# Kernel optimization log

Measured on AMD Instinct MI355X. Metric: run time of the kernel, lower is better.

The kernel has to match this reference:

```python
import jax, jax.numpy as jnp
import numpy as np

N = 50000
E = 800000
IN_DIM, HID, OUT, DW = 128, 96, 40, 64
N_LBL = 10


def _deg_inv_sqrt(dst, n):
    # PyG gcn_norm: degree over target nodes of (A + I)
    deg = jax.ops.segment_sum(jnp.ones((dst.shape[0],), jnp.float32), dst, num_segments=n) + 1.0
    return jnp.where(deg > 0, 1.0 / jnp.sqrt(deg), 0.0)


def gcn_conv(h_in, W, b, src, dst, dinv):
    # GCNConv: out = D^-1/2 (A + I) D^-1/2 (X W) + b
    h = h_in @ W                                  # [N, F]
    norm = (dinv[src] * dinv[dst])[:, None]       # [E, 1]
    agg = jax.ops.segment_sum(h[src] * norm, dst, num_segments=h.shape[0])
    agg = agg + h * (dinv * dinv)[:, None]        # self-loop term
    return agg + b


def setup_inputs() -> dict:
    key = jax.random.key(0)
    ks = jax.random.split(key, 12)
    inp = {
        "x": jax.random.normal(ks[0], (N, IN_DIM), jnp.float32),
        "y": jax.random.uniform(ks[1], (N, OUT), jnp.float32),
        "edge_index": jax.random.randint(ks[2], (2, E), 0, N, jnp.int64 if jax.config.read("jax_enable_x64") else jnp.int32),
        "deep_walk_emb": jax.random.normal(ks[3], (N, DW), jnp.float32),
        # learned params
        "W_gcn1": jax.random.normal(ks[4], (IN_DIM, HID), jnp.float32) * (1.0 / np.sqrt(IN_DIM)),
        "b_gcn1": jnp.zeros((HID,), jnp.float32),
        "W_gcn2": jax.random.normal(ks[5], (HID, HID), jnp.float32) * (1.0 / np.sqrt(HID)),
        "b_gcn2": jnp.zeros((HID,), jnp.float32),
        "W_lbl": jax.random.normal(ks[6], (N_LBL, OUT, OUT), jnp.float32) * (1.0 / np.sqrt(OUT)),
        "b_lbl": jnp.zeros((N_LBL, OUT), jnp.float32),
        "W_fuse": jax.random.normal(ks[7], (HID + OUT + DW, OUT), jnp.float32) * (1.0 / np.sqrt(HID + OUT + DW)),
        "b_fuse": jnp.zeros((OUT,), jnp.float32),
    }
    return inp


def reference(x, y, edge_index, deep_walk_emb,
              W_gcn1, b_gcn1, W_gcn2, b_gcn2,
              W_lbl, b_lbl, W_fuse, b_fuse):
    src, dst = edge_index[0], edge_index[1]
    dinv = _deg_inv_sqrt(dst, x.shape[0])

    # feature propagation: 2 stacked GCNConv layers
    h = gcn_conv(x, W_gcn1, b_gcn1, src, dst, dinv)
    h = gcn_conv(h, W_gcn2, b_gcn2, src, dst, dinv)

    # label propagation: 10 stacked GCNConv layers via scan over stacked weights
    def step(carry, wb):
        W, b = wb
        return gcn_conv(carry, W, b, src, dst, dinv), None

    x_label, _ = jax.lax.scan(step, y, (W_lbl, b_lbl))

    fused = jnp.concatenate([h, x_label, deep_walk_emb], axis=1)  # [N, HID+OUT+DW]
    out = fused @ W_fuse + b_fuse
    return jax.nn.sigmoid(out)
```

## Files before the change

### kernel.cpp

```cpp
#include <hip/hip_runtime.h>
#include <hip/hip_bf16.h>
#include <math.h>

#define THREADS 256
typedef _Float16 h16;

__device__ __forceinline__ void ld8h(const h16* p, float* f) {
    union { uint4 u; h16 h[8]; } c;
    c.u = *(const uint4*)p;
#pragma unroll
    for (int j = 0; j < 8; ++j) f[j] = (float)c.h[j];
}

__global__ __launch_bounds__(256) void count_part_kernel(
    const int* __restrict__ dst, int* __restrict__ cnt, int E, int n)
{
    const int cls = blockIdx.x & 7;
    const int nb  = gridDim.x >> 3;
    const int sub = blockIdx.x >> 3;
    const int lo = (int)((long long)n * cls / 8);
    const int hi = (int)((long long)n * (cls + 1) / 8);
    const int stride = nb * 256;
    for (int e = sub * 256 + threadIdx.x; e < E; e += stride) {
        int d = dst[e];
        if (d >= lo && d < hi) atomicAdd(&cnt[d], 1);
    }
}

__global__ __launch_bounds__(256) void scatter_part_kernel(
    const int* __restrict__ src, const int* __restrict__ dst,
    int* __restrict__ cursor, int* __restrict__ col, int E, int n)
{
    const int cls = blockIdx.x & 7;
    const int nb  = gridDim.x >> 3;
    const int sub = blockIdx.x >> 3;
    const int lo = (int)((long long)n * cls / 8);
    const int hi = (int)((long long)n * (cls + 1) / 8);
    const int stride = nb * 256;
    for (int e = sub * 256 + threadIdx.x; e < E; e += stride) {
        int d = dst[e];
        if (d >= lo && d < hi) {
            int p = atomicAdd(&cursor[d], 1);
            col[p] = src[e];
        }
    }
}

__global__ __launch_bounds__(256) void scanp1_pre_kernel(
    const int* __restrict__ cnt, int* __restrict__ partial, int n, int NB,
    const float* __restrict__ Wl, const float* __restrict__ bl,
    const float* __restrict__ W1, const float* __restrict__ W2,
    const float* __restrict__ b1,
    float* __restrict__ C0, float* __restrict__ betas,
    float* __restrict__ W12, float* __restrict__ betaf1)
{
    __shared__ __align__(16) float smem[9216];
    const int tid = threadIdx.x;
    const int bid = blockIdx.x;

    if (bid < NB) {
        int* red = (int*)smem;
        int base = bid * 1024 + tid * 4;
        int s = 0;
        if (base + 3 < n) {
            int4 v = *(const int4*)(cnt + base);
            s = v.x + v.y + v.z + v.w;
        } else {
            for (int k = 0; k < 4; k++) { int i = base + k; if (i < n) s += cnt[i]; }
        }
        red[tid] = s;
        __syncthreads();
        for (int off = 128; off > 0; off >>= 1) {
            if (tid < off) red[tid] += red[tid + off];
            __syncthreads();
        }
        if (tid == 0) partial[bid] = red[0];
        return;
    }

    if (bid == NB) {
        float* Ca  = smem;
        float* Cb  = smem + 1600;
        float* sWm = smem + 3200;
        float* bls = smem + 4800;
        for (int idx = tid; idx < 100; idx += 256)
            ((float4*)bls)[idx] = ((const float4*)bl)[idx];
        for (int idx = tid; idx < 1600; idx += 256)
            Ca[idx] = ((idx / 40) == (idx % 40)) ? 1.f : 0.f;
        if (tid < 40) betas[9 * 40 + tid] = bl[9 * 40 + tid];
        __syncthreads();
        float* cur = Ca;
        float* nxt = Cb;
        for (int m = 9; m >= 0; --m) {
            for (int idx = tid; idx < 400; idx += 256)
                ((float4*)sWm)[idx] = ((const float4*)(Wl + (size_t)m * 1600))[idx];
            __syncthreads();
            for (int sid = tid; sid < 400; sid += 256) {
                int i = sid / 10, jq = sid - (sid / 10) * 10;
                const float* wr = &sWm[i * 40];
                const float4* c4 = (const float4*)cur;
                float4 a = make_float4(0.f, 0.f, 0.f, 0.f);
#pragma unroll
                for (int k = 0; k < 40; ++k) {
                    float w = wr[k];
                    float4 c = c4[k * 10 + jq];
                    a.x = fmaf(w, c.x, a.x); a.y = fmaf(w, c.y, a.y);
                    a.z = fmaf(w, c.z, a.z); a.w = fmaf(w, c.w, a.w);
                }
                ((float4*)nxt)[sid] = a;
            }
            __syncthreads();
            if (m >= 1 && tid < 40) {
                float s = 0.f;
                const float* br = &bls[(m - 1) * 40];
#pragma unroll
                for (int k = 0; k < 40; ++k) s = fmaf(br[k], nxt[k * 40 + tid], s);
                betas[(size_t)(m - 1) * 40 + tid] = s;
            }
            float* t = cur; cur = nxt; nxt = t;
            __syncthreads();
        }
        for (int idx = tid; idx < 1600; idx += 256) C0[idx] = cur[idx];
        return;
    }

    float* sW2 = smem;
    for (int idx = tid; idx < 2304; idx += 256)
        ((float4*)sW2)[idx] = ((const float4*)W2)[idx];
    __syncthreads();
    int idx = (bid - NB - 1) * 256 + tid;
    {
        int i = idx / 96, j = idx - (idx / 96) * 96;
        float s = 0.f;
        const float* wr = W1 + (size_t)i * 96;
#pragma unroll 8
        for (int k = 0; k < 96; ++k) s = fmaf(wr[k], sW2[k * 96 + j], s);
        W12[idx] = s;
    }
    if (bid == NB + 1 && tid < 96) {
        float s = 0.f;
        for (int k = 0; k < 96; ++k) s = fmaf(b1[k], sW2[k * 96 + tid], s);
        betaf1[tid] = s;
    }
}

__global__ __launch_bounds__(256) void scan_p2(int* __restrict__ partial, int* __restrict__ rowptr, int nb, int n) {
    __shared__ int sm[256];
    int tid = threadIdx.x;
    int v = (tid < nb) ? partial[tid] : 0;
    sm[tid] = v;
    __syncthreads();
    int acc = v;
    for (int off = 1; off < 256; off <<= 1) {
        int t = (tid >= off) ? sm[tid - off] : 0;
        __syncthreads();
        acc += t;
        sm[tid] = acc;
        __syncthreads();
    }
    if (tid < nb) partial[tid] = acc - v;
    if (tid == 255) rowptr[n] = sm[255];
}

__global__ __launch_bounds__(256) void scan_p3(const int* __restrict__ cnt, const int* __restrict__ partial,
                                               int* __restrict__ rowptr, int* __restrict__ cursor,
                                               float* __restrict__ dinv, int n) {
    __shared__ int tsum[256];
    int tid = threadIdx.x;
    int base = blockIdx.x * 1024 + tid * 4;
    int v0 = 0, v1 = 0, v2 = 0, v3 = 0;
    if (base + 3 < n) {
        int4 t = *(const int4*)(cnt + base);
        v0 = t.x; v1 = t.y; v2 = t.z; v3 = t.w;
    } else {
        if (base + 0 < n) v0 = cnt[base + 0];
        if (base + 1 < n) v1 = cnt[base + 1];
        if (base + 2 < n) v2 = cnt[base + 2];
        if (base + 3 < n) v3 = cnt[base + 3];
    }
    int s = v0 + v1 + v2 + v3;
    tsum[tid] = s;
    __syncthreads();
    int acc = s;
    for (int off = 1; off < 256; off <<= 1) {
        int t = (tid >= off) ? tsum[tid - off] : 0;
        __syncthreads();
        acc += t;
        tsum[tid] = acc;
        __syncthreads();
    }
    int run = partial[blockIdx.x] + acc - s;
    int vv[4] = {v0, v1, v2, v3};
    for (int k = 0; k < 4; k++) {
        int i = base + k;
        if (i < n) {
            rowptr[i] = run; cursor[i] = run; run += vv[k];
            dinv[i] = rsqrtf((float)vv[k] + 1.0f);
        }
    }
}

template<int FIN, int FOUT, typename TX>
__device__ __forceinline__ void gemm_body(
    const TX* __restrict__ X, const float* __restrict__ W,
    const float* __restrict__ dinv, h16* __restrict__ Y, int n,
    float* sX, float* sW, int bid, int tid)
{
    constexpr int KC = (FIN % 32 == 0) ? 32 : FIN;
    constexpr int NCHUNK = FIN / KC;
    constexpr int TN = (FOUT + 15) / 16;
    constexpr int BM = 64;
    constexpr int KP = KC + 4;

    const int tj = tid & 15;
    const int ti = tid >> 4;
    const int i0 = bid * BM;

    float acc[4][TN] = {};

    for (int c = 0; c < NCHUNK; ++c) {
        const int k0 = c * KC;
        __syncthreads();
        if constexpr (sizeof(TX) == 2) {
            constexpr int K8 = KC / 8;
            for (int v = tid; v < BM * K8; v += 256) {
                int r = v / K8, q = v - r * K8;
                int gi = i0 + r;
                float f[8] = {0.f, 0.f, 0.f, 0.f, 0.f, 0.f, 0.f, 0.f};
                if (gi < n) ld8h((const h16*)X + (size_t)gi * FIN + k0 + q * 8, f);
                float* p = &sX[r * KP + q * 8];
#pragma unroll
                for (int j = 0; j < 8; ++j) p[j] = f[j];
            }
        } else {
            constexpr int K4 = KC / 4;
            for (int v = tid; v < BM * K4; v += 256) {
                int r = v / K4, q = v - r * K4;
                int gi = i0 + r;
                float4 val = (gi < n) ? *(const float4*)((const float*)X + (size_t)gi * FIN + k0 + q * 4)
                                      : make_float4(0.f, 0.f, 0.f, 0.f);
                float* p = &sX[r * KP + q * 4];
                p[0] = val.x; p[1] = val.y; p[2] = val.z; p[3] = val.w;
            }
        }
        for (int v = tid; v < KC * FOUT; v += 256) {
            int kk = v / FOUT;
            int j = v - kk * FOUT;
            sW[j * KP + kk] = W[(size_t)(k0 + kk) * FOUT + j];
        }
        __syncthreads();
#pragma unroll
        for (int kk = 0; kk < KC; kk += 4) {
            float4 xv[4];
#pragma unroll
            for (int m = 0; m < 4; ++m)
                xv[m] = *(const float4*)&sX[(ti + 16 * m) * KP + kk];
#pragma unroll
            for (int u = 0; u < TN; ++u) {
                float4 wv = *(const float4*)&sW[(tj + 16 * u) * KP + kk];
#pragma unroll
                for (int m = 0; m < 4; ++m) {
                    acc[m][u] = fmaf(xv[m].x, wv.x, acc[m][u]);
                    acc[m][u] = fmaf(xv[m].y, wv.y, acc[m][u]);
                    acc[m][u] = fmaf(xv[m].z, wv.z, acc[m][u]);
                    acc[m][u] = fmaf(xv[m].w, wv.w, acc[m][u]);
                }
            }
        }
    }

#pragma unroll
    for (int m = 0; m < 4; ++m) {
        int gi = i0 + ti + 16 * m;
        if (gi >= n) continue;
        float dv = dinv[gi];
#pragma unroll
        for (int u = 0; u < TN; ++u) {
            int j = tj + 16 * u;
            if (j < FOUT) Y[(size_t)gi * FOUT + j] = (h16)(acc[m][u] * dv);
        }
    }
}

template<int FIN, int FOUT, typename TX>
__global__ __launch_bounds__(256) void gemm_kernel(
    const TX* __restrict__ X, const float* __restrict__ W,
    const float* __restrict__ dinv, h16* __restrict__ Y, int n)
{
    constexpr int KC = (FIN % 32 == 0) ? 32 : FIN;
    constexpr int KP = KC + 4;
    constexpr int TN = (FOUT + 15) / 16;
    __shared__ __align__(16) float smem[64 * KP + TN * 16 * KP];
    gemm_body<FIN, FOUT, TX>(X, W, dinv, Y, n, smem, smem + 64 * KP, blockIdx.x, threadIdx.x);
}

template<int F, int PRE>
__device__ __forceinline__ void agg_body(
    const h16* __restrict__ hs, const int* __restrict__ rowptr,
    const int* __restrict__ col, const float* __restrict__ dinv,
    const float* __restrict__ bias, h16* __restrict__ out, int n,
    int bid, int tid)
{
    constexpr int F8 = F / 8;
    int gt = bid * 256 + tid;
    if (gt >= n * F8) return;
    int i = gt / F8;
    int f = gt - i * F8;
    int s = rowptr[i], e = rowptr[i + 1];
    const h16* base = hs + (size_t)f * 8;
    float acc[8];
    ld8h(hs + (size_t)i * F + f * 8, acc);
    int k = s;
    for (; k + 8 <= e; k += 8) {
        int c[8];
        union { uint4 u; h16 h[8]; } a[8];
#pragma unroll
        for (int q = 0; q < 8; ++q) c[q] = col[k + q];
#pragma unroll
        for (int q = 0; q < 8; ++q) a[q].u = *(const uint4*)(base + (size_t)c[q] * F);
#pragma unroll
        for (int j = 0; j < 8; ++j) {
            float t0 = ((float)a[0].h[j] + (float)a[1].h[j]) + ((float)a[2].h[j] + (float)a[3].h[j]);
            float t1 = ((float)a[4].h[j] + (float)a[5].h[j]) + ((float)a[6].h[j] + (float)a[7].h[j]);
            acc[j] += t0 + t1;
        }
    }
    for (; k + 4 <= e; k += 4) {
        int c0 = col[k], c1 = col[k + 1], c2 = col[k + 2], c3 = col[k + 3];
        union { uint4 u; h16 h[8]; } a0, a1, a2, a3;
        a0.u = *(const uint4*)(base + (size_t)c0 * F);
        a1.u = *(const uint4*)(base + (size_t)c1 * F);
        a2.u = *(const uint4*)(base + (size_t)c2 * F);
        a3.u = *(const uint4*)(base + (size_t)c3 * F);
#pragma unroll
        for (int j = 0; j < 8; ++j)
            acc[j] += ((float)a0.h[j] + (float)a1.h[j]) + ((float)a2.h[j] + (float)a3.h[j]);
    }
    for (; k < e; k++) {
        float v[8];
        ld8h(base + (size_t)col[k] * F, v);
#pragma unroll
        for (int j = 0; j < 8; ++j) acc[j] += v[j];
    }
    float dv = dinv[i];
    float sc = PRE ? dv : 1.f;
    union { uint4 u; h16 h[8]; } o;
#pragma unroll
    for (int j = 0; j < 8; ++j) o.h[j] = (h16)((acc[j] * dv + bias[f * 8 + j]) * sc);
    *(uint4*)(out + (size_t)i * F + f * 8) = o.u;
}

template<int F, int PRE>
__global__ __launch_bounds__(256) void agg_h(
    const h16* __restrict__ hs, const int* __restrict__ rowptr,
    const int* __restrict__ col, const float* __restrict__ dinv,
    const float* __restrict__ bias, h16* __restrict__ out, int n) {
    agg_body<F, PRE>(hs, rowptr, col, dinv, bias, out, n, blockIdx.x, threadIdx.x);
}

template<int PRE2>
__global__ __launch_bounds__(256) void agg_dual_kernel(
    const h16* __restrict__ hsA, const float* __restrict__ biasA, h16* __restrict__ outA,
    const h16* __restrict__ hsB, const float* __restrict__ biasB, h16* __restrict__ outB,
    const int* __restrict__ rowptr, const int* __restrict__ col,
    const float* __restrict__ dinv, int n, int nblkA)
{
    if (blockIdx.x < nblkA)
        agg_body<40, 1>(hsA, rowptr, col, dinv, biasA, outA, n, blockIdx.x, threadIdx.x);
    else
        agg_body<96, PRE2>(hsB, rowptr, col, dinv, biasB, outB, n, blockIdx.x - nblkA, threadIdx.x);
}

template<int KC, typename T>
__device__ __forceinline__ void fuse_chunk(
    const T* __restrict__ src, int FIN, int k0, int wrow0,
    const float* __restrict__ Wf, float* sX, float* sW,
    float acc[4][3], int i0, int n, int tid)
{
    constexpr int KP = 44;
    __syncthreads();
    if constexpr (sizeof(T) == 2) {
        constexpr int K8 = KC / 8;
        for (int v = tid; v < 64 * K8; v += 256) {
            int r = v / K8, q = v - r * K8;
            int gi = i0 + r;
            float f[8] = {0.f, 0.f, 0.f, 0.f, 0.f, 0.f, 0.f, 0.f};
            if (gi < n) ld8h((const h16*)src + (size_t)gi * FIN + k0 + q * 8, f);
            float* p = &sX[r * KP + q * 8];
#pragma unroll
            for (int j = 0; j < 8; ++j) p[j] = f[j];
        }
    } else {
        constexpr int K4 = KC / 4;
        for (int v = tid; v < 64 * K4; v += 256) {
            int r = v / K4, q = v - r * K4;
            int gi = i0 + r;
            float4 val = (gi < n) ? *(const float4*)((const float*)src + (size_t)gi * FIN + k0 + q * 4)
                                  : make_float4(0.f, 0.f, 0.f, 0.f);
            float* p = &sX[r * KP + q * 4];
            p[0] = val.x; p[1] = val.y; p[2] = val.z; p[3] = val.w;
        }
    }
    for (int v = tid; v < KC * 40; v += 256) {
        int kk = v / 40, j = v - kk * 40;
        sW[j * KP + kk] = Wf[(size_t)(wrow0 + kk) * 40 + j];
    }
    __syncthreads();
    int tj = tid & 15, ti = tid >> 4;
#pragma unroll
    for (int kk = 0; kk < KC; kk += 4) {
        float4 xv[4];
#pragma unroll
        for (int m = 0; m < 4; ++m)
            xv[m] = *(const float4*)&sX[(ti + 16 * m) * KP + kk];
#pragma unroll
        for (int u = 0; u < 3; ++u) {
            float4 wv = *(const float4*)&sW[(tj + 16 * u) * KP + kk];
#pragma unroll
            for (int m = 0; m < 4; ++m) {
                acc[m][u] = fmaf(xv[m].x, wv.x, acc[m][u]);
                acc[m][u] = fmaf(xv[m].y, wv.y, acc[m][u]);
                acc[m][u] = fmaf(xv[m].z, wv.z, acc[m][u]);
                acc[m][u] = fmaf(xv[m].w, wv.w, acc[m][u]);
            }
        }
    }
}

__global__ __launch_bounds__(256) void fuse_gemm_kernel(
    const h16* __restrict__ h2, const h16* __restrict__ xl,
    const float* __restrict__ dw, const float* __restrict__ Wf,
    const float* __restrict__ bf, float* __restrict__ out, int n)
{
    __shared__ __align__(16) float sX[64 * 44];
    __shared__ __align__(16) float sW[48 * 44];
    float acc[4][3] = {};
    const int tid = threadIdx.x;
    const int i0 = blockIdx.x * 64;
    fuse_chunk<32>(h2, 96, 0,  0,   Wf, sX, sW, acc, i0, n, tid);
    fuse_chunk<32>(h2, 96, 32, 32,  Wf, sX, sW, acc, i0, n, tid);
    fuse_chunk<32>(h2, 96, 64, 64,  Wf, sX, sW, acc, i0, n, tid);
    fuse_chunk<40>(xl, 40, 0,  96,  Wf, sX, sW, acc, i0, n, tid);
    fuse_chunk<32>(dw, 64, 0,  136, Wf, sX, sW, acc, i0, n, tid);
    fuse_chunk<32>(dw, 64, 32, 168, Wf, sX, sW, acc, i0, n, tid);
    const int tj = tid & 15, ti = tid >> 4;
#pragma unroll
    for (int m = 0; m < 4; ++m) {
        int gi = i0 + ti + 16 * m;
        if (gi >= n) continue;
#pragma unroll
        for (int u = 0; u < 3; ++u) {
            int j = tj + 16 * u;
            if (j < 40) {
                float t = acc[m][u] + bf[j];
                out[(size_t)gi * 40 + j] = 1.f / (1.f + expf(-t));
            }
        }
    }
}

extern "C" void kernel_launch(void* const* d_in, const int* in_sizes, int n_in,
                              void* d_out, int out_size, void* d_ws, size_t ws_size,
                              hipStream_t stream) {
    const float* x   = (const float*)d_in[0];
    const float* y   = (const float*)d_in[1];
    const int*   ei  = (const int*)d_in[2];
    const float* dwe = (const float*)d_in[3];
    const float* W1  = (const float*)d_in[4];
    const float* b1  = (const float*)d_in[5];
    const float* W2  = (const float*)d_in[6];
    const float* b2  = (const float*)d_in[7];
    const float* Wl  = (const float*)d_in[8];
    const float* bl  = (const float*)d_in[9];
    const float* Wf  = (const float*)d_in[10];
    const float* bf  = (const float*)d_in[11];
    float* out = (float*)d_out;

    const int n = in_sizes[0] / 128;
    const int E = in_sizes[2] / 2;
    const int* srcp = ei;
    const int* dstp = ei + E;

    char* ws = (char*)d_ws;
    size_t off = 0;
    auto alloc = [&](size_t bytes) -> void* {
        void* p = ws + off;
        off += bytes;
        off = (off + 255) & ~(size_t)255;
        return p;
    };

    int*   cnt     = (int*)alloc((size_t)n * 4);
    float* dinv    = (float*)alloc((size_t)n * 4);
    int*   rowptr  = (int*)alloc((size_t)(n + 1) * 4);
    int*   cursor  = (int*)alloc((size_t)n * 4);
    int*   partial = (int*)alloc(256 * 4);
    int*   col     = (int*)alloc((size_t)E * 4);
    h16*   A96     = (h16*)alloc((size_t)n * 96 * 2);
    h16*   B96     = (h16*)alloc((size_t)n * 96 * 2);
    h16*   Z0      = (h16*)alloc((size_t)n * 40 * 2);
    h16*   LA      = (h16*)alloc((size_t)n * 40 * 2);
    h16*   LB      = (h16*)alloc((size_t)n * 40 * 2);
    float* C0      = (float*)alloc(1600 * 4);
    float* betas   = (float*)alloc(10 * 40 * 4);
    float* W12     = (float*)alloc(128 * 96 * 4);
    float* betaf1  = (float*)alloc(96 * 4);
    (void)ws_size;

    const int NB      = (n + 1023) / 1024;
    const int gb_gm   = (n + 63) / 64;
    const int gb_a96  = (n * 12 + THREADS - 1) / THREADS;
    const int gb_a40  = (n * 5 + THREADS - 1) / THREADS;
    const int PART_BLOCKS = 2048;

    hipMemsetAsync(cnt, 0, (size_t)n * 4, stream);
    count_part_kernel<<<PART_BLOCKS, THREADS, 0, stream>>>(dstp, cnt, E, n);
    scanp1_pre_kernel<<<NB + 49, THREADS, 0, stream>>>(
        cnt, partial, n, NB, Wl, bl, W1, W2, b1, C0, betas, W12, betaf1);
    scan_p2<<<1, THREADS, 0, stream>>>(partial, rowptr, NB, n);
    scan_p3<<<NB, THREADS, 0, stream>>>(cnt, partial, rowptr, cursor, dinv, n);
    scatter_part_kernel<<<PART_BLOCKS, THREADS, 0, stream>>>(srcp, dstp, cursor, col, E, n);

    gemm_kernel<40, 40, float><<<gb_gm, THREADS, 0, stream>>>(y, C0, dinv, Z0, n);
    gemm_kernel<128, 96, float><<<gb_gm, THREADS, 0, stream>>>(x, W12, dinv, A96, n);

    agg_dual_kernel<1><<<gb_a40 + gb_a96, THREADS, 0, stream>>>(
        Z0, betas + 0, LA, A96, betaf1, B96, rowptr, col, dinv, n, gb_a40);
    agg_dual_kernel<0><<<gb_a40 + gb_a96, THREADS, 0, stream>>>(
        LA, betas + 40, LB, B96, b2, A96, rowptr, col, dinv, n, gb_a40);

    const h16* cur = LB;
    const h16* xl = LB;
    for (int m = 3; m <= 10; m++) {
        h16* nxt = (m & 1) ? LA : LB;
        if (m < 10)
            agg_h<40, 1><<<gb_a40, THREADS, 0, stream>>>(cur, rowptr, col, dinv, betas + (size_t)(m - 1) * 40, nxt, n);
        else
            agg_h<40, 0><<<gb_a40, THREADS, 0, stream>>>(cur, rowptr, col, dinv, betas + (size_t)(m - 1) * 40, nxt, n);
        cur = nxt;
        xl = nxt;
    }

    fuse_gemm_kernel<<<gb_gm, THREADS, 0, stream>>>(A96, xl, dwe, Wf, bf, out, n);
}
```

Measured before the change: 386.5 us.

## Merge aggregation layers into one cooperative persistent kernel with grid syncs

Replaces ten separate aggregation kernel launches (two dual-feature and eight label-propagation launches) with a single cooperative kernel. It uses a persistent grid sized from occupancy and separates layers with grid.sync(). The aim is to cut per-launch overhead and the gaps between dependent layers. The cost is grid-wide barrier latency, possibly lower occupancy, and a grid-stride loop over work blocks.

```diff
diff --git a/kernel.cpp b/kernel.cpp
--- a/kernel.cpp
+++ b/kernel.cpp
@@ -1,6 +1,9 @@
 #include <hip/hip_runtime.h>
 #include <hip/hip_bf16.h>
+#include <hip/hip_cooperative_groups.h>
 #include <math.h>
+
+namespace cg = cooperative_groups;
 
 #define THREADS 256
 typedef _Float16 h16;
@@ -350,25 +353,41 @@
     *(uint4*)(out + (size_t)i * F + f * 8) = o.u;
 }
 
-template<int F, int PRE>
-__global__ __launch_bounds__(256) void agg_h(
-    const h16* __restrict__ hs, const int* __restrict__ rowptr,
-    const int* __restrict__ col, const float* __restrict__ dinv,
-    const float* __restrict__ bias, h16* __restrict__ out, int n) {
-    agg_body<F, PRE>(hs, rowptr, col, dinv, bias, out, n, blockIdx.x, threadIdx.x);
-}
-
-template<int PRE2>
-__global__ __launch_bounds__(256) void agg_dual_kernel(
-    const h16* __restrict__ hsA, const float* __restrict__ biasA, h16* __restrict__ outA,
-    const h16* __restrict__ hsB, const float* __restrict__ biasB, h16* __restrict__ outB,
+__global__ __launch_bounds__(256) void agg_coop_kernel(
+    const h16* __restrict__ Z0, h16* __restrict__ LA, h16* __restrict__ LB,
+    h16* __restrict__ A96, h16* __restrict__ B96,
+    const float* __restrict__ betas, const float* __restrict__ betaf1,
+    const float* __restrict__ b2,
     const int* __restrict__ rowptr, const int* __restrict__ col,
-    const float* __restrict__ dinv, int n, int nblkA)
-{
-    if (blockIdx.x < nblkA)
-        agg_body<40, 1>(hsA, rowptr, col, dinv, biasA, outA, n, blockIdx.x, threadIdx.x);
-    else
-        agg_body<96, PRE2>(hsB, rowptr, col, dinv, biasB, outB, n, blockIdx.x - nblkA, threadIdx.x);
+    const float* __restrict__ dinv, int n, int nblkL, int nblkF)
+{
+    cg::grid_group grid = cg::this_grid();
+    const int G = gridDim.x;
+    const int tid = threadIdx.x;
+
+    for (int w = blockIdx.x; w < nblkL + nblkF; w += G) {
+        if (w < nblkL) agg_body<40, 1>(Z0, rowptr, col, dinv, betas, LA, n, w, tid);
+        else           agg_body<96, 1>(A96, rowptr, col, dinv, betaf1, B96, n, w - nblkL, tid);
+    }
+    grid.sync();
+    for (int w = blockIdx.x; w < nblkL + nblkF; w += G) {
+        if (w < nblkL) agg_body<40, 1>(LA, rowptr, col, dinv, betas + 40, LB, n, w, tid);
+        else           agg_body<96, 0>(B96, rowptr, col, dinv, b2, A96, n, w - nblkL, tid);
+    }
+    const h16* cur = LB;
+    for (int m = 3; m <= 10; ++m) {
+        grid.sync();
+        h16* nxt = (m & 1) ? LA : LB;
+        const float* beta = betas + (size_t)(m - 1) * 40;
+        if (m < 10) {
+            for (int w = blockIdx.x; w < nblkL; w += G)
+                agg_body<40, 1>(cur, rowptr, col, dinv, beta, nxt, n, w, tid);
+        } else {
+            for (int w = blockIdx.x; w < nblkL; w += G)
+                agg_body<40, 0>(cur, rowptr, col, dinv, beta, nxt, n, w, tid);
+        }
+        cur = nxt;
+    }
 }
 
 template<int KC, typename T>
@@ -524,22 +543,30 @@
     gemm_kernel<40, 40, float><<<gb_gm, THREADS, 0, stream>>>(y, C0, dinv, Z0, n);
     gemm_kernel<128, 96, float><<<gb_gm, THREADS, 0, stream>>>(x, W12, dinv, A96, n);
 
-    agg_dual_kernel<1><<<gb_a40 + gb_a96, THREADS, 0, stream>>>(
-        Z0, betas + 0, LA, A96, betaf1, B96, rowptr, col, dinv, n, gb_a40);
-    agg_dual_kernel<0><<<gb_a40 + gb_a96, THREADS, 0, stream>>>(
-        LA, betas + 40, LB, B96, b2, A96, rowptr, col, dinv, n, gb_a40);
-
-    const h16* cur = LB;
-    const h16* xl = LB;
-    for (int m = 3; m <= 10; m++) {
-        h16* nxt = (m & 1) ? LA : LB;
-        if (m < 10)
-            agg_h<40, 1><<<gb_a40, THREADS, 0, stream>>>(cur, rowptr, col, dinv, betas + (size_t)(m - 1) * 40, nxt, n);
-        else
-            agg_h<40, 0><<<gb_a40, THREADS, 0, stream>>>(cur, rowptr, col, dinv, betas + (size_t)(m - 1) * 40, nxt, n);
-        cur = nxt;
-        xl = nxt;
-    }
-
-    fuse_gemm_kernel<<<gb_gm, THREADS, 0, stream>>>(A96, xl, dwe, Wf, bf, out, n);
-}
+    {
+        int perCU = 0;
+        hipError_t oe = hipOccupancyMaxActiveBlocksPerMultiprocessor(
+            &perCU, (const void*)agg_coop_kernel, THREADS, 0);
+        if (oe != hipSuccess || perCU <= 0) perCU = 4;
+        int grid = perCU * 256;
+        int maxwork = gb_a40 + gb_a96;
+        if (grid > maxwork) grid = maxwork;
+
+        const h16* z0c = Z0;
+        h16 *laP = LA, *lbP = LB, *a96P = A96, *b96P = B96;
+        const float *betasP = betas, *betaf1P = betaf1, *b2P = b2;
+        const int *rowptrP = rowptr, *colP = col;
+        const float* dinvP = dinv;
+        int nv = n, nblkL = gb_a40, nblkF = gb_a96;
+        void* cargs[] = {
+            (void*)&z0c, (void*)&laP, (void*)&lbP, (void*)&a96P, (void*)&b96P,
+            (void*)&betasP, (void*)&betaf1P, (void*)&b2P,
+            (void*)&rowptrP, (void*)&colP, (void*)&dinvP,
+            (void*)&nv, (void*)&nblkL, (void*)&nblkF
+        };
+        hipLaunchCooperativeKernel((const void*)agg_coop_kernel,
+                                   dim3(grid), dim3(THREADS), cargs, 0, stream);
+    }
+
+    fuse_gemm_kernel<<<gb_gm, THREADS, 0, stream>>>(A96, LB, dwe, Wf, bf, out, n);
+}
```

Result: slower. 982.4 us (+154.2%).

## Fold fusion weights into GCN chains so all propagation runs at width 40

Applied to the files above, without the earlier changes.

Pushes the final fusion matrix Wf back through both linear chains. The feature path is precomputed as W1·W2·Wf1, and the label chain product is folded into Wf's label block, so both GCN branches aggregate 40-wide half-precision features instead of 96-wide. The deepwalk projection is done by a separate small GEMM and added during the second hop, and the final fusion GEMM is replaced by a sigmoid epilogue in the last aggregation. This cuts gather bandwidth and removes the fuse kernel, at the cost of a longer serial weight-precompute block and changed rounding order.

```diff
diff --git a/kernel.cpp b/kernel.cpp
--- a/kernel.cpp
+++ b/kernel.cpp
@@ -49,12 +49,12 @@
 __global__ __launch_bounds__(256) void scanp1_pre_kernel(
     const int* __restrict__ cnt, int* __restrict__ partial, int n, int NB,
     const float* __restrict__ Wl, const float* __restrict__ bl,
-    const float* __restrict__ W1, const float* __restrict__ W2,
-    const float* __restrict__ b1,
-    float* __restrict__ C0, float* __restrict__ betas,
-    float* __restrict__ W12, float* __restrict__ betaf1)
-{
-    __shared__ __align__(16) float smem[9216];
+    const float* __restrict__ W2, const float* __restrict__ b1,
+    const float* __restrict__ b2, const float* __restrict__ Wf,
+    float* __restrict__ CM, float* __restrict__ betas,
+    float* __restrict__ T, float* __restrict__ betaf1p, float* __restrict__ b2p)
+{
+    __shared__ __align__(16) float smem[13200];
     const int tid = threadIdx.x;
     const int bid = blockIdx.x;
 
@@ -78,88 +78,121 @@
         return;
     }
 
-    if (bid == NB) {
-        float* Ca  = smem;
-        float* Cb  = smem + 1600;
-        float* sWm = smem + 3200;
-        float* bls = smem + 4800;
-        for (int idx = tid; idx < 100; idx += 256)
-            ((float4*)bls)[idx] = ((const float4*)bl)[idx];
-        for (int idx = tid; idx < 1600; idx += 256)
-            Ca[idx] = ((idx / 40) == (idx % 40)) ? 1.f : 0.f;
-        if (tid < 40) betas[9 * 40 + tid] = bl[9 * 40 + tid];
-        __syncthreads();
-        float* cur = Ca;
-        float* nxt = Cb;
-        for (int m = 9; m >= 0; --m) {
-            for (int idx = tid; idx < 400; idx += 256)
-                ((float4*)sWm)[idx] = ((const float4*)(Wl + (size_t)m * 1600))[idx];
-            __syncthreads();
-            for (int sid = tid; sid < 400; sid += 256) {
-                int i = sid / 10, jq = sid - (sid / 10) * 10;
-                const float* wr = &sWm[i * 40];
-                const float4* c4 = (const float4*)cur;
-                float4 a = make_float4(0.f, 0.f, 0.f, 0.f);
-#pragma unroll
-                for (int k = 0; k < 40; ++k) {
-                    float w = wr[k];
-                    float4 c = c4[k * 10 + jq];
-                    a.x = fmaf(w, c.x, a.x); a.y = fmaf(w, c.y, a.y);
-                    a.z = fmaf(w, c.z, a.z); a.w = fmaf(w, c.w, a.w);
-                }
-                ((float4*)nxt)[sid] = a;
+    float* Ca  = smem;
+    float* Cb  = smem + 1600;
+    float* sWm = smem + 3200;
+    float* bls = smem + 4800;
+    for (int idx = tid; idx < 100; idx += 256)
+        ((float4*)bls)[idx] = ((const float4*)bl)[idx];
+    for (int idx = tid; idx < 400; idx += 256)
+        ((float4*)Ca)[idx] = ((const float4*)(Wf + 3840))[idx];
+    __syncthreads();
+    if (tid < 40) {
+        float s = 0.f;
+#pragma unroll
+        for (int k = 0; k < 40; ++k) s = fmaf(bls[360 + k], Ca[k * 40 + tid], s);
+        betas[360 + tid] = s;
+    }
+    __syncthreads();
+    float* cur = Ca;
+    float* nxt = Cb;
+    for (int m = 9; m >= 0; --m) {
+        for (int idx = tid; idx < 400; idx += 256)
+            ((float4*)sWm)[idx] = ((const float4*)(Wl + (size_t)m * 1600))[idx];
+        __syncthreads();
+        for (int sid = tid; sid < 400; sid += 256) {
+            int i = sid / 10, jq = sid - (sid / 10) * 10;
+            const float* wr = &sWm[i * 40];
+            const float4* c4 = (const float4*)cur;
+            float4 a = make_float4(0.f, 0.f, 0.f, 0.f);
+#pragma unroll
+            for (int k = 0; k < 40; ++k) {
+                float w = wr[k];
+                float4 c = c4[k * 10 + jq];
+                a.x = fmaf(w, c.x, a.x); a.y = fmaf(w, c.y, a.y);
+                a.z = fmaf(w, c.z, a.z); a.w = fmaf(w, c.w, a.w);
             }
-            __syncthreads();
-            if (m >= 1 && tid < 40) {
-                float s = 0.f;
-                const float* br = &bls[(m - 1) * 40];
-#pragma unroll
-                for (int k = 0; k < 40; ++k) s = fmaf(br[k], nxt[k * 40 + tid], s);
-                betas[(size_t)(m - 1) * 40 + tid] = s;
-            }
-            float* t = cur; cur = nxt; nxt = t;
-            __syncthreads();
-        }
-        for (int idx = tid; idx < 1600; idx += 256) C0[idx] = cur[idx];
-        return;
-    }
-
-    float* sW2 = smem;
+            ((float4*)nxt)[sid] = a;
+        }
+        __syncthreads();
+        if (m >= 1 && tid < 40) {
+            float s = 0.f;
+            const float* br = &bls[(m - 1) * 40];
+#pragma unroll
+            for (int k = 0; k < 40; ++k) s = fmaf(br[k], nxt[k * 40 + tid], s);
+            betas[(size_t)(m - 1) * 40 + tid] = s;
+        }
+        float* t = cur; cur = nxt; nxt = t;
+        __syncthreads();
+    }
+    for (int idx = tid; idx < 1600; idx += 256) CM[idx] = cur[idx];
+    __syncthreads();
+
+    float* sW2  = smem;
+    float* sWf1 = smem + 9216;
+    float* vq   = smem + 13056;
     for (int idx = tid; idx < 2304; idx += 256)
         ((float4*)sW2)[idx] = ((const float4*)W2)[idx];
-    __syncthreads();
-    int idx = (bid - NB - 1) * 256 + tid;
-    {
-        int i = idx / 96, j = idx - (idx / 96) * 96;
+    for (int idx = tid; idx < 960; idx += 256)
+        ((float4*)sWf1)[idx] = ((const float4*)Wf)[idx];
+    __syncthreads();
+    for (int idx = tid; idx < 3840; idx += 256) {
+        int k = idx / 40, j = idx - (idx / 40) * 40;
         float s = 0.f;
-        const float* wr = W1 + (size_t)i * 96;
 #pragma unroll 8
-        for (int k = 0; k < 96; ++k) s = fmaf(wr[k], sW2[k * 96 + j], s);
-        W12[idx] = s;
-    }
-    if (bid == NB + 1 && tid < 96) {
+        for (int q = 0; q < 96; ++q) s = fmaf(sW2[k * 96 + q], sWf1[q * 40 + j], s);
+        T[idx] = s;
+    }
+    if (tid < 96) {
         float s = 0.f;
         for (int k = 0; k < 96; ++k) s = fmaf(b1[k], sW2[k * 96 + tid], s);
-        betaf1[tid] = s;
-    }
-}
-
-__global__ __launch_bounds__(256) void scan_p2(int* __restrict__ partial, int* __restrict__ rowptr, int nb, int n) {
-    __shared__ int sm[256];
-    int tid = threadIdx.x;
-    int v = (tid < nb) ? partial[tid] : 0;
-    sm[tid] = v;
-    __syncthreads();
-    int acc = v;
-    for (int off = 1; off < 256; off <<= 1) {
-        int t = (tid >= off) ? sm[tid - off] : 0;
-        __syncthreads();
-        acc += t;
-        sm[tid] = acc;
-        __syncthreads();
-    }
-    if (tid < nb) partial[tid] = acc - v;
-    if (tid == 255) rowptr[n] = sm[255];
+        vq[tid] = s;
+    }
+    __syncthreads();
+    if (tid < 40) {
+        float s1 = 0.f, s2 = 0.f;
+        for (int q = 0; q < 96; ++q) {
+            float w = sWf1[q * 40 + tid];
+            s1 = fmaf(vq[q], w, s1);
+            s2 = fmaf(b2[q], w, s2);
+        }
+        betaf1p[tid] = s1;
+        b2p[tid] = s2;
+    }
+}
+
+__global__ __launch_bounds__(256) void scanp2_wf_kernel(
+    int* __restrict__ partial, int* __restrict__ rowptr, int nb, int n,
+    const float* __restrict__ W1, const float* __restrict__ T, float* __restrict__ WF)
+{
+    __shared__ __align__(16) float smem[3840];
+    const int tid = threadIdx.x;
+    if (blockIdx.x == 0) {
+        int* sm = (int*)smem;
+        int v = (tid < nb) ? partial[tid] : 0;
+        sm[tid] = v;
+        __syncthreads();
+        int acc = v;
+        for (int off = 1; off < 256; off <<= 1) {
+            int t = (tid >= off) ? sm[tid - off] : 0;
+            __syncthreads();
+            acc += t;
+            sm[tid] = acc;
+            __syncthreads();
+        }
+        if (tid < nb) partial[tid] = acc - v;
+        if (tid == 255) rowptr[n] = sm[255];
+        return;
+    }
+    for (int idx = tid; idx < 960; idx += 256)
+        ((float4*)smem)[idx] = ((const float4*)T)[idx];
+    __syncthreads();
+    int idx = (blockIdx.x - 1) * 256 + tid;
+    int i = idx / 40, j = idx - (idx / 40) * 40;
+    float s = 0.f;
+#pragma unroll 8
+    for (int k = 0; k < 96; ++k) s = fmaf(W1[(size_t)i * 96 + k], smem[k * 40 + j], s);
+    WF[idx] = s;
 }
 
 __global__ __launch_bounds__(256) void scan_p3(const int* __restrict__ cnt, const int* __restrict__ partial,
@@ -200,21 +233,25 @@
     }
 }
 
-template<int FIN, int FOUT, typename TX>
-__device__ __forceinline__ void gemm_body(
+template<int FIN, int FOUT, typename TX, typename TO, int DODINV>
+__global__ __launch_bounds__(256) void gemm_kernel(
     const TX* __restrict__ X, const float* __restrict__ W,
-    const float* __restrict__ dinv, h16* __restrict__ Y, int n,
-    float* sX, float* sW, int bid, int tid)
+    const float* __restrict__ dinv, TO* __restrict__ Y, int n)
 {
     constexpr int KC = (FIN % 32 == 0) ? 32 : FIN;
     constexpr int NCHUNK = FIN / KC;
     constexpr int TN = (FOUT + 15) / 16;
+    constexpr int FOUTP = TN * 16;
     constexpr int BM = 64;
     constexpr int KP = KC + 4;
 
+    __shared__ __align__(16) float sX[BM * KP];
+    __shared__ __align__(16) float sW[FOUTP * KP];
+
+    const int tid = threadIdx.x;
     const int tj = tid & 15;
     const int ti = tid >> 4;
-    const int i0 = bid * BM;
+    const int i0 = blockIdx.x * BM;
 
     float acc[4][TN] = {};
 
@@ -273,33 +310,26 @@
     for (int m = 0; m < 4; ++m) {
         int gi = i0 + ti + 16 * m;
         if (gi >= n) continue;
-        float dv = dinv[gi];
+        float dv = 1.f;
+        if constexpr (DODINV) dv = dinv[gi];
 #pragma unroll
         for (int u = 0; u < TN; ++u) {
             int j = tj + 16 * u;
-            if (j < FOUT) Y[(size_t)gi * FOUT + j] = (h16)(acc[m][u] * dv);
-        }
-    }
-}
-
-template<int FIN, int FOUT, typename TX>
-__global__ __launch_bounds__(256) void gemm_kernel(
-    const TX* __restrict__ X, const float* __restrict__ W,
-    const float* __restrict__ dinv, h16* __restrict__ Y, int n)
-{
-    constexpr int KC = (FIN % 32 == 0) ? 32 : FIN;
-    constexpr int KP = KC + 4;
-    constexpr int TN = (FOUT + 15) / 16;
-    __shared__ __align__(16) float smem[64 * KP + TN * 16 * KP];
-    gemm_body<FIN, FOUT, TX>(X, W, dinv, Y, n, smem, smem + 64 * KP, blockIdx.x, threadIdx.x);
-}
-
-template<int F, int PRE>
+            if (j < FOUT) Y[(size_t)gi * FOUT + j] = (TO)(acc[m][u] * dv);
+        }
+    }
+}
+
+template<int F, int MODE>
 __device__ __forceinline__ void agg_body(
     const h16* __restrict__ hs, const int* __restrict__ rowptr,
     const int* __restrict__ col, const float* __restrict__ dinv,
     const float* __restrict__ bias, h16* __restrict__ out, int n,
-    int bid, int tid)
+    int bid, int tid,
+    const float* __restrict__ extra32 = nullptr,
+    const h16* __restrict__ f2 = nullptr,
+    const float* __restrict__ bfp = nullptr,
+    float* __restrict__ outf = nullptr)
 {
     constexpr int F8 = F / 8;
     int gt = bid * 256 + tid;
@@ -343,23 +373,43 @@
         for (int j = 0; j < 8; ++j) acc[j] += v[j];
     }
     float dv = dinv[i];
-    float sc = PRE ? dv : 1.f;
-    union { uint4 u; h16 h[8]; } o;
-#pragma unroll
-    for (int j = 0; j < 8; ++j) o.h[j] = (h16)((acc[j] * dv + bias[f * 8 + j]) * sc);
-    *(uint4*)(out + (size_t)i * F + f * 8) = o.u;
-}
-
-template<int F, int PRE>
-__global__ __launch_bounds__(256) void agg_h(
+    if constexpr (MODE == 3) {
+        float fv[8];
+        ld8h(f2 + (size_t)i * F + f * 8, fv);
+        float r[8];
+#pragma unroll
+        for (int j = 0; j < 8; ++j) {
+            float t = acc[j] * dv + bias[f * 8 + j] + fv[j] + bfp[f * 8 + j];
+            r[j] = 1.f / (1.f + expf(-t));
+        }
+        float* po = outf + (size_t)i * F + f * 8;
+        *(float4*)po       = make_float4(r[0], r[1], r[2], r[3]);
+        *(float4*)(po + 4) = make_float4(r[4], r[5], r[6], r[7]);
+    } else if constexpr (MODE == 2) {
+        const float* pe = extra32 + (size_t)i * F + f * 8;
+        float4 e0 = *(const float4*)pe;
+        float4 e1 = *(const float4*)(pe + 4);
+        float ex[8] = {e0.x, e0.y, e0.z, e0.w, e1.x, e1.y, e1.z, e1.w};
+        union { uint4 u; h16 h[8]; } o;
+#pragma unroll
+        for (int j = 0; j < 8; ++j) o.h[j] = (h16)(acc[j] * dv + bias[f * 8 + j] + ex[j]);
+        *(uint4*)(out + (size_t)i * F + f * 8) = o.u;
+    } else {
+        union { uint4 u; h16 h[8]; } o;
+#pragma unroll
+        for (int j = 0; j < 8; ++j) o.h[j] = (h16)((acc[j] * dv + bias[f * 8 + j]) * dv);
+        *(uint4*)(out + (size_t)i * F + f * 8) = o.u;
+    }
+}
+
+__global__ __launch_bounds__(256) void agg40_pre_kernel(
     const h16* __restrict__ hs, const int* __restrict__ rowptr,
     const int* __restrict__ col, const float* __restrict__ dinv,
     const float* __restrict__ bias, h16* __restrict__ out, int n) {
-    agg_body<F, PRE>(hs, rowptr, col, dinv, bias, out, n, blockIdx.x, threadIdx.x);
-}
-
-template<int PRE2>
-__global__ __launch_bounds__(256) void agg_dual_kernel(
+    agg_body<40, 1>(hs, rowptr, col, dinv, bias, out, n, blockIdx.x, threadIdx.x);
+}
+
+__global__ __launch_bounds__(256) void agg_hop1_kernel(
     const h16* __restrict__ hsA, const float* __restrict__ biasA, h16* __restrict__ outA,
     const h16* __restrict__ hsB, const float* __restrict__ biasB, h16* __restrict__ outB,
     const int* __restrict__ rowptr, const int* __restrict__ col,
@@ -368,95 +418,30 @@
     if (blockIdx.x < nblkA)
         agg_body<40, 1>(hsA, rowptr, col, dinv, biasA, outA, n, blockIdx.x, threadIdx.x);
     else
-        agg_body<96, PRE2>(hsB, rowptr, col, dinv, biasB, outB, n, blockIdx.x - nblkA, threadIdx.x);
-}
-
-template<int KC, typename T>
-__device__ __forceinline__ void fuse_chunk(
-    const T* __restrict__ src, int FIN, int k0, int wrow0,
-    const float* __restrict__ Wf, float* sX, float* sW,
-    float acc[4][3], int i0, int n, int tid)
-{
-    constexpr int KP = 44;
-    __syncthreads();
-    if constexpr (sizeof(T) == 2) {
-        constexpr int K8 = KC / 8;
-        for (int v = tid; v < 64 * K8; v += 256) {
-            int r = v / K8, q = v - r * K8;
-            int gi = i0 + r;
-            float f[8] = {0.f, 0.f, 0.f, 0.f, 0.f, 0.f, 0.f, 0.f};
-            if (gi < n) ld8h((const h16*)src + (size_t)gi * FIN + k0 + q * 8, f);
-            float* p = &sX[r * KP + q * 8];
-#pragma unroll
-            for (int j = 0; j < 8; ++j) p[j] = f[j];
-        }
-    } else {
-        constexpr int K4 = KC / 4;
-        for (int v = tid; v < 64 * K4; v += 256) {
-            int r = v / K4, q = v - r * K4;
-            int gi = i0 + r;
-            float4 val = (gi < n) ? *(const float4*)((const float*)src + (size_t)gi * FIN + k0 + q * 4)
-                                  : make_float4(0.f, 0.f, 0.f, 0.f);
-            float* p = &sX[r * KP + q * 4];
-            p[0] = val.x; p[1] = val.y; p[2] = val.z; p[3] = val.w;
-        }
-    }
-    for (int v = tid; v < KC * 40; v += 256) {
-        int kk = v / 40, j = v - kk * 40;
-        sW[j * KP + kk] = Wf[(size_t)(wrow0 + kk) * 40 + j];
-    }
-    __syncthreads();
-    int tj = tid & 15, ti = tid >> 4;
-#pragma unroll
-    for (int kk = 0; kk < KC; kk += 4) {
-        float4 xv[4];
-#pragma unroll
-        for (int m = 0; m < 4; ++m)
-            xv[m] = *(const float4*)&sX[(ti + 16 * m) * KP + kk];
-#pragma unroll
-        for (int u = 0; u < 3; ++u) {
-            float4 wv = *(const float4*)&sW[(tj + 16 * u) * KP + kk];
-#pragma unroll
-            for (int m = 0; m < 4; ++m) {
-                acc[m][u] = fmaf(xv[m].x, wv.x, acc[m][u]);
-                acc[m][u] = fmaf(xv[m].y, wv.y, acc[m][u]);
-                acc[m][u] = fmaf(xv[m].z, wv.z, acc[m][u]);
-                acc[m][u] = fmaf(xv[m].w, wv.w, acc[m][u]);
-            }
-        }
-    }
-}
-
-__global__ __launch_bounds__(256) void fuse_gemm_kernel(
-    const h16* __restrict__ h2, const h16* __restrict__ xl,
-    const float* __restrict__ dw, const float* __restrict__ Wf,
-    const float* __restrict__ bf, float* __restrict__ out, int n)
-{
-    __shared__ __align__(16) float sX[64 * 44];
-    __shared__ __align__(16) float sW[48 * 44];
-    float acc[4][3] = {};
-    const int tid = threadIdx.x;
-    const int i0 = blockIdx.x * 64;
-    fuse_chunk<32>(h2, 96, 0,  0,   Wf, sX, sW, acc, i0, n, tid);
-    fuse_chunk<32>(h2, 96, 32, 32,  Wf, sX, sW, acc, i0, n, tid);
-    fuse_chunk<32>(h2, 96, 64, 64,  Wf, sX, sW, acc, i0, n, tid);
-    fuse_chunk<40>(xl, 40, 0,  96,  Wf, sX, sW, acc, i0, n, tid);
-    fuse_chunk<32>(dw, 64, 0,  136, Wf, sX, sW, acc, i0, n, tid);
-    fuse_chunk<32>(dw, 64, 32, 168, Wf, sX, sW, acc, i0, n, tid);
-    const int tj = tid & 15, ti = tid >> 4;
-#pragma unroll
-    for (int m = 0; m < 4; ++m) {
-        int gi = i0 + ti + 16 * m;
-        if (gi >= n) continue;
-#pragma unroll
-        for (int u = 0; u < 3; ++u) {
-            int j = tj + 16 * u;
-            if (j < 40) {
-                float t = acc[m][u] + bf[j];
-                out[(size_t)gi * 40 + j] = 1.f / (1.f + expf(-t));
-            }
-        }
-    }
+        agg_body<40, 1>(hsB, rowptr, col, dinv, biasB, outB, n, blockIdx.x - nblkA, threadIdx.x);
+}
+
+__global__ __launch_bounds__(256) void agg_hop2_kernel(
+    const h16* __restrict__ hsA, const float* __restrict__ biasA, h16* __restrict__ outA,
+    const h16* __restrict__ hsB, const float* __restrict__ biasB, h16* __restrict__ outB,
+    const float* __restrict__ dw40,
+    const int* __restrict__ rowptr, const int* __restrict__ col,
+    const float* __restrict__ dinv, int n, int nblkA)
+{
+    if (blockIdx.x < nblkA)
+        agg_body<40, 1>(hsA, rowptr, col, dinv, biasA, outA, n, blockIdx.x, threadIdx.x);
+    else
+        agg_body<40, 2>(hsB, rowptr, col, dinv, biasB, outB, n, blockIdx.x - nblkA, threadIdx.x, dw40);
+}
+
+__global__ __launch_bounds__(256) void agg_final_kernel(
+    const h16* __restrict__ hs, const int* __restrict__ rowptr,
+    const int* __restrict__ col, const float* __restrict__ dinv,
+    const float* __restrict__ bias, const h16* __restrict__ f2,
+    const float* __restrict__ bf, float* __restrict__ outf, int n)
+{
+    agg_body<40, 3>(hs, rowptr, col, dinv, bias, nullptr, n, blockIdx.x, threadIdx.x,
+                    nullptr, f2, bf, outf);
 }
 
 extern "C" void kernel_launch(void* const* d_in, const int* in_sizes, int n_in,
@@ -496,50 +481,51 @@
     int*   cursor  = (int*)alloc((size_t)n * 4);
     int*   partial = (int*)alloc(256 * 4);
     int*   col     = (int*)alloc((size_t)E * 4);
-    h16*   A96     = (h16*)alloc((size_t)n * 96 * 2);
-    h16*   B96     = (h16*)alloc((size_t)n * 96 * 2);
     h16*   Z0      = (h16*)alloc((size_t)n * 40 * 2);
     h16*   LA      = (h16*)alloc((size_t)n * 40 * 2);
     h16*   LB      = (h16*)alloc((size_t)n * 40 * 2);
-    float* C0      = (float*)alloc(1600 * 4);
+    h16*   F0      = (h16*)alloc((size_t)n * 40 * 2);
+    h16*   FB      = (h16*)alloc((size_t)n * 40 * 2);
+    h16*   F2      = (h16*)alloc((size_t)n * 40 * 2);
+    float* DW40    = (float*)alloc((size_t)n * 40 * 4);
+    float* CM      = (float*)alloc(1600 * 4);
     float* betas   = (float*)alloc(10 * 40 * 4);
-    float* W12     = (float*)alloc(128 * 96 * 4);
-    float* betaf1  = (float*)alloc(96 * 4);
+    float* T       = (float*)alloc(96 * 40 * 4);
+    float* WF      = (float*)alloc(128 * 40 * 4);
+    float* betaf1p = (float*)alloc(40 * 4);
+    float* b2p     = (float*)alloc(40 * 4);
     (void)ws_size;
 
     const int NB      = (n + 1023) / 1024;
     const int gb_gm   = (n + 63) / 64;
-    const int gb_a96  = (n * 12 + THREADS - 1) / THREADS;
     const int gb_a40  = (n * 5 + THREADS - 1) / THREADS;
     const int PART_BLOCKS = 2048;
 
     hipMemsetAsync(cnt, 0, (size_t)n * 4, stream);
     count_part_kernel<<<PART_BLOCKS, THREADS, 0, stream>>>(dstp, cnt, E, n);
-    scanp1_pre_kernel<<<NB + 49, THREADS, 0, stream>>>(
-        cnt, partial, n, NB, Wl, bl, W1, W2, b1, C0, betas, W12, betaf1);
-    scan_p2<<<1, THREADS, 0, stream>>>(partial, rowptr, NB, n);
+    scanp1_pre_kernel<<<NB + 1, THREADS, 0, stream>>>(
+        cnt, partial, n, NB, Wl, bl, W2, b1, b2, Wf, CM, betas, T, betaf1p, b2p);
+    scanp2_wf_kernel<<<21, THREADS, 0, stream>>>(partial, rowptr, NB, n, W1, T, WF);
     scan_p3<<<NB, THREADS, 0, stream>>>(cnt, partial, rowptr, cursor, dinv, n);
     scatter_part_kernel<<<PART_BLOCKS, THREADS, 0, stream>>>(srcp, dstp, cursor, col, E, n);
 
-    gemm_kernel<40, 40, float><<<gb_gm, THREADS, 0, stream>>>(y, C0, dinv, Z0, n);
-    gemm_kernel<128, 96, float><<<gb_gm, THREADS, 0, stream>>>(x, W12, dinv, A96, n);
-
-    agg_dual_kernel<1><<<gb_a40 + gb_a96, THREADS, 0, stream>>>(
-        Z0, betas + 0, LA, A96, betaf1, B96, rowptr, col, dinv, n, gb_a40);
-    agg_dual_kernel<0><<<gb_a40 + gb_a96, THREADS, 0, stream>>>(
-        LA, betas + 40, LB, B96, b2, A96, rowptr, col, dinv, n, gb_a40);
+    gemm_kernel<40, 40, float, h16, 1><<<gb_gm, THREADS, 0, stream>>>(y, CM, dinv, Z0, n);
+    gemm_kernel<128, 40, float, h16, 1><<<gb_gm, THREADS, 0, stream>>>(x, WF, dinv, F0, n);
+    gemm_kernel<64, 40, float, float, 0><<<gb_gm, THREADS, 0, stream>>>(dwe, Wf + 136 * 40, nullptr, DW40, n);
+
+    agg_hop1_kernel<<<2 * gb_a40, THREADS, 0, stream>>>(
+        Z0, betas + 0, LA, F0, betaf1p, FB, rowptr, col, dinv, n, gb_a40);
+    agg_hop2_kernel<<<2 * gb_a40, THREADS, 0, stream>>>(
+        LA, betas + 40, LB, FB, b2p, F2, DW40, rowptr, col, dinv, n, gb_a40);
 
     const h16* cur = LB;
-    const h16* xl = LB;
-    for (int m = 3; m <= 10; m++) {
+    for (int m = 3; m <= 9; m++) {
         h16* nxt = (m & 1) ? LA : LB;
-        if (m < 10)
-            agg_h<40, 1><<<gb_a40, THREADS, 0, stream>>>(cur, rowptr, col, dinv, betas + (size_t)(m - 1) * 40, nxt, n);
-        else
-            agg_h<40, 0><<<gb_a40, THREADS, 0, stream>>>(cur, rowptr, col, dinv, betas + (size_t)(m - 1) * 40, nxt, n);
+        agg40_pre_kernel<<<gb_a40, THREADS, 0, stream>>>(
+            cur, rowptr, col, dinv, betas + (size_t)(m - 1) * 40, nxt, n);
         cur = nxt;
-        xl = nxt;
-    }
-
-    fuse_gemm_kernel<<<gb_gm, THREADS, 0, stream>>>(A96, xl, dwe, Wf, bf, out, n);
-}
+    }
+
+    agg_final_kernel<<<gb_a40, THREADS, 0, stream>>>(
+        cur, rowptr, col, dinv, betas + 9 * 40, F2, bf, out, n);
+}
```

New measurement: 363.4 us. -6.0%, faster.
